# Kernel tuning notes

Measured on AMD Instinct MI355X. Metric: run time of the kernel, lower is better.

Reference implementation:

```python
import jax, jax.numpy as jnp
import numpy as np


def setup_inputs() -> dict:
    key = jax.random.key(0)
    ks = jax.random.split(key, 5)
    B, T, I, H = 32, 2048, 512, 512
    s_i = 1.0 / np.sqrt(I)
    s_h = 1.0 / np.sqrt(H)
    return {
        "x": jax.random.normal(ks[0], (B, T, I), dtype=jnp.float32),
        "Wi": jax.random.normal(ks[1], (4 * H, I), dtype=jnp.float32) * s_i,
        "bi": jax.random.normal(ks[2], (4 * H,), dtype=jnp.float32) * s_i,
        "Wh": jax.random.normal(ks[3], (4 * H, H), dtype=jnp.float32) * s_h,
        "bh": jax.random.normal(ks[4], (4 * H,), dtype=jnp.float32) * s_h,
    }


def reference(x, Wi, bi, Wh, bh):
    # x: [B, T, I] (batch_first). Wi: [4H, I], Wh: [4H, H].
    B, T, I = x.shape
    H = Wh.shape[1]
    # Precompute input contribution for all timesteps in one GEMM: [T, B, 4H]
    gx = jnp.einsum('bti,gi->tbg', x, Wi) + bi + bh

    def step(carry, g):
        h, c = carry
        gates = g + h @ Wh.T  # [B, 4H]
        i_g, f_g, c_g, o_g = jnp.split(gates, 4, axis=1)
        c_new = jax.nn.sigmoid(f_g) * c + jax.nn.sigmoid(i_g) * jnp.tanh(c_g)
        h_new = jax.nn.sigmoid(o_g) * jnp.tanh(c_new)
        return (h_new, c_new), h_new

    h0 = jnp.zeros((B, H), dtype=x.dtype)
    c0 = jnp.zeros((B, H), dtype=x.dtype)
    (h_fin, c_fin), ys = jax.lax.scan(step, (h0, c0), gx)
    output = ys.transpose(1, 0, 2)  # [B, T, H] (batch_first)
    return output, h_fin, c_fin
```

## Files before the change

kernel.cpp:

```cpp
#include <hip/hip_runtime.h>
#include <hip/hip_bf16.h>

typedef unsigned short ushort_t;
typedef __attribute__((ext_vector_type(8))) short bf16x8;
typedef __attribute__((ext_vector_type(4))) float f32x4;
typedef __attribute__((ext_vector_type(2))) float f32x2;

#define B_SZ 32
#define T_SZ 2048
#define I_SZ 512
#define H_SZ 512
#define G_SZ 2048
#define T_C  64
#define N_CHUNK (T_SZ / T_C)

__device__ __forceinline__ ushort_t f2bf(float f) {
    union { float f; unsigned u32; } c; c.f = f;
    unsigned r = c.u32 + 0x7fffu + ((c.u32 >> 16) & 1u);
    return (ushort_t)(r >> 16);
}
__device__ __forceinline__ bf16x8 cvt8(const float* __restrict__ p) {
    f32x4 a = *(const f32x4*)p;
    f32x4 b = *(const f32x4*)(p + 4);
    bf16x8 v;
    v[0] = (short)f2bf(a[0]); v[1] = (short)f2bf(a[1]);
    v[2] = (short)f2bf(a[2]); v[3] = (short)f2bf(a[3]);
    v[4] = (short)f2bf(b[0]); v[5] = (short)f2bf(b[1]);
    v[6] = (short)f2bf(b[2]); v[7] = (short)f2bf(b[3]);
    return v;
}
__device__ __forceinline__ float sigf(float x) { return 1.0f / (1.0f + __expf(-x)); }
__device__ __forceinline__ float tanh_fast(float x) {
    float a = fabsf(x);
    float e = __expf(-2.0f * a);
    float t = (1.0f - e) / (1.0f + e);
    return x < 0.0f ? -t : t;
}

__global__ __launch_bounds__(256) void gemm_gx(
    const float* __restrict__ X,
    const float* __restrict__ Wi,
    const float* __restrict__ bi,
    const float* __restrict__ bh,
    float* __restrict__ gx,
    int t0)
{
    __shared__ ushort_t As[128][40];
    __shared__ ushort_t Bs[128][40];

    const int tid  = threadIdx.x;
    const int lane = tid & 63;
    const int wv   = tid >> 6;
    const int wm   = (wv >> 1) * 64;
    const int wn   = (wv & 1) * 64;
    const int m0   = blockIdx.y * 128;
    const int n0   = blockIdx.x * 128;

    f32x4 acc[4][4];
#pragma unroll
    for (int i = 0; i < 4; i++)
#pragma unroll
        for (int j = 0; j < 4; j++) acc[i][j] = (f32x4)0.0f;

    const int lrow   = tid >> 2;
    const int lchunk = (tid & 3) * 8;

    const int m1 = m0 + lrow, m2 = m1 + 64;
    const size_t xr1 = ((size_t)(m1 >> 6) * T_SZ + t0 + (m1 & (T_C - 1))) * 512;
    const size_t xr2 = ((size_t)(m2 >> 6) * T_SZ + t0 + (m2 & (T_C - 1))) * 512;

    for (int kk = 0; kk < 512; kk += 32) {
        *(bf16x8*)&As[lrow][lchunk]      = cvt8(X + xr1 + kk + lchunk);
        *(bf16x8*)&As[lrow + 64][lchunk] = cvt8(X + xr2 + kk + lchunk);
        const float* bp = Wi + (size_t)(n0 + lrow) * 512 + kk + lchunk;
        *(bf16x8*)&Bs[lrow][lchunk]      = cvt8(bp);
        *(bf16x8*)&Bs[lrow + 64][lchunk] = cvt8(bp + (size_t)64 * 512);
        __syncthreads();

        const int koff = (lane >> 4) * 8;
        const int rsel = lane & 15;
        bf16x8 af[4], bfr[4];
#pragma unroll
        for (int mt = 0; mt < 4; mt++) af[mt]  = *(const bf16x8*)&As[wm + mt * 16 + rsel][koff];
#pragma unroll
        for (int nt = 0; nt < 4; nt++) bfr[nt] = *(const bf16x8*)&Bs[wn + nt * 16 + rsel][koff];
#pragma unroll
        for (int mt = 0; mt < 4; mt++)
#pragma unroll
            for (int nt = 0; nt < 4; nt++)
                acc[mt][nt] = __builtin_amdgcn_mfma_f32_16x16x32_bf16(af[mt], bfr[nt], acc[mt][nt], 0, 0, 0);
        __syncthreads();
    }

    const int rsel = lane & 15;
    const int rq   = (lane >> 4) * 4;
#pragma unroll
    for (int nt = 0; nt < 4; nt++) {
        const int n = n0 + wn + nt * 16 + rsel;
        const float bias = bi[n] + bh[n];
#pragma unroll
        for (int mt = 0; mt < 4; mt++) {
#pragma unroll
            for (int r = 0; r < 4; r++) {
                const int m  = m0 + wm + mt * 16 + rq + r;
                const int b  = m >> 6;
                const int tc = m & (T_C - 1);
                gx[((size_t)tc * B_SZ + b) * G_SZ + n] = acc[mt][nt][r] + bias;
            }
        }
    }
}

__global__ __launch_bounds__(256) void lstm_scan(
    const float* __restrict__ Wh,
    const float* __restrict__ gx,
    float* __restrict__ out,
    ushort_t* __restrict__ hstate,
    float*    __restrict__ cstate,
    unsigned* __restrict__ flags,
    int t0)
{
    const int w    = blockIdx.x;
    const int hb   = w * 16;
    const int tid  = threadIdx.x;
    const int lane = tid & 63;
    const int g    = tid >> 6;
    const int rsel = lane & 15;
    const int quad = lane >> 4;

    __shared__ float gs[4][32][16];

    bf16x8 bfrag[16];
    {
        const float* wp = Wh + (size_t)(g * 512 + hb + rsel) * 512 + quad * 8;
#pragma unroll
        for (int kt = 0; kt < 16; kt++) bfrag[kt] = cvt8(wp + kt * 32);
    }

    const int eb = tid >> 3;
    const int eh = (tid & 7) * 2;
    const size_t cidx = (size_t)eb * 512 + hb + eh;
    float c0 = 0.0f, c1 = 0.0f;
    if (t0 > 0) { c0 = cstate[cidx]; c1 = cstate[cidx + 1]; }
    float h0 = 0.0f, h1 = 0.0f;
    const size_t out_base = (size_t)eb * (T_SZ * H_SZ) + hb + eh;

    for (int tl = 0; tl < T_C; tl++) {
        const int t = t0 + tl;

        float gl0[4], gl1[4];
        {
            const float* gp = gx + (size_t)tl * (B_SZ * G_SZ) + (size_t)(g * 512 + hb + rsel);
#pragma unroll
            for (int r = 0; r < 4; r++) {
                const int b0 = quad * 4 + r;
                gl0[r] = gp[(size_t)b0 * G_SZ];
                gl1[r] = gp[(size_t)(b0 + 16) * G_SZ];
            }
        }
        __builtin_amdgcn_sched_barrier(0);

        if (t > 0) {
            const unsigned tgt = (unsigned)t;
            for (;;) {
                unsigned f = __hip_atomic_load(&flags[(lane & 31) * 32],
                                               __ATOMIC_RELAXED, __HIP_MEMORY_SCOPE_AGENT);
                if (__all((int)(f >= tgt))) break;
            }
            __builtin_amdgcn_fence(__ATOMIC_ACQUIRE, "agent");
        }

        f32x4 acc0a = (f32x4)0.0f, acc0b = (f32x4)0.0f;
        f32x4 acc1a = (f32x4)0.0f, acc1b = (f32x4)0.0f;
        if (t > 0) {
            const ushort_t* hp = hstate + (size_t)(t & 1) * (B_SZ * H_SZ)
                                 + (size_t)rsel * 512 + quad * 8;
#pragma unroll
            for (int kt = 0; kt < 16; kt += 2) {
                bf16x8 a0 = *(const bf16x8*)(hp + kt * 32);
                bf16x8 a1 = *(const bf16x8*)(hp + (size_t)16 * 512 + kt * 32);
                bf16x8 a2 = *(const bf16x8*)(hp + (kt + 1) * 32);
                bf16x8 a3 = *(const bf16x8*)(hp + (size_t)16 * 512 + (kt + 1) * 32);
                acc0a = __builtin_amdgcn_mfma_f32_16x16x32_bf16(a0, bfrag[kt],     acc0a, 0, 0, 0);
                acc1a = __builtin_amdgcn_mfma_f32_16x16x32_bf16(a1, bfrag[kt],     acc1a, 0, 0, 0);
                acc0b = __builtin_amdgcn_mfma_f32_16x16x32_bf16(a2, bfrag[kt + 1], acc0b, 0, 0, 0);
                acc1b = __builtin_amdgcn_mfma_f32_16x16x32_bf16(a3, bfrag[kt + 1], acc1b, 0, 0, 0);
            }
        }
        const f32x4 acc0 = acc0a + acc0b;
        const f32x4 acc1 = acc1a + acc1b;

#pragma unroll
        for (int r = 0; r < 4; r++) {
            const int b0 = quad * 4 + r;
            gs[g][b0][rsel]      = acc0[r] + gl0[r];
            gs[g][b0 + 16][rsel] = acc1[r] + gl1[r];
        }
        __syncthreads();

        {
            const float ig0 = gs[0][eb][eh], ig1 = gs[0][eb][eh + 1];
            const float fg0 = gs[1][eb][eh], fg1 = gs[1][eb][eh + 1];
            const float cg0 = gs[2][eb][eh], cg1 = gs[2][eb][eh + 1];
            const float og0 = gs[3][eb][eh], og1 = gs[3][eb][eh + 1];
            c0 = sigf(fg0) * c0 + sigf(ig0) * tanh_fast(cg0);
            c1 = sigf(fg1) * c1 + sigf(ig1) * tanh_fast(cg1);
            h0 = sigf(og0) * tanh_fast(c0);
            h1 = sigf(og1) * tanh_fast(c1);
            const unsigned hpack = (unsigned)f2bf(h0) | ((unsigned)f2bf(h1) << 16);
            ushort_t* wrp = hstate + (size_t)((t + 1) & 1) * (B_SZ * H_SZ) + cidx;
            __hip_atomic_store((unsigned*)wrp, hpack, __ATOMIC_RELAXED, __HIP_MEMORY_SCOPE_AGENT);
        }
        __syncthreads();

        if (tid == 0)
            __hip_atomic_store(&flags[w * 32], (unsigned)(t + 1),
                               __ATOMIC_RELEASE, __HIP_MEMORY_SCOPE_AGENT);

        f32x2 ho; ho[0] = h0; ho[1] = h1;
        *(f32x2*)(out + out_base + (size_t)t * H_SZ) = ho;
    }

    cstate[cidx] = c0; cstate[cidx + 1] = c1;
    if (t0 + T_C == T_SZ) {
        float* hf = out + (size_t)B_SZ * T_SZ * H_SZ;
        f32x2 hv; hv[0] = h0; hv[1] = h1;
        *(f32x2*)(hf + cidx) = hv;
        float* cf = hf + B_SZ * H_SZ;
        f32x2 cv; cv[0] = c0; cv[1] = c1;
        *(f32x2*)(cf + cidx) = cv;
    }
}

extern "C" void kernel_launch(void* const* d_in, const int* in_sizes, int n_in,
                              void* d_out, int out_size, void* d_ws, size_t ws_size,
                              hipStream_t stream) {
    const float* x  = (const float*)d_in[0];
    const float* Wi = (const float*)d_in[1];
    const float* bi = (const float*)d_in[2];
    const float* Wh = (const float*)d_in[3];
    const float* bh = (const float*)d_in[4];
    float* out = (float*)d_out;

    const size_t GX_BYTES = (size_t)T_C * B_SZ * G_SZ * sizeof(float);
    float*    gxc    = (float*)d_ws;
    ushort_t* hstate = (ushort_t*)((char*)d_ws + GX_BYTES);
    float*    cstate = (float*)   ((char*)d_ws + GX_BYTES + 65536);
    unsigned* flags  = (unsigned*)((char*)d_ws + GX_BYTES + 65536 + 65536);

    hipMemsetAsync(flags, 0, 4096, stream);

    for (int k = 0; k < N_CHUNK; k++) {
        const int t0 = k * T_C;
        gemm_gx<<<dim3(G_SZ / 128, (B_SZ * T_C) / 128), dim3(256), 0, stream>>>(
            x, Wi, bi, bh, gxc, t0);
        lstm_scan<<<dim3(32), dim3(256), 0, stream>>>(Wh, gxc, out, hstate, cstate, flags, t0);
    }
}
```

Before: 14.25 ms.

## Give each scan wave all four gates to drop block barriers and LDS exchange

The recurrent scan is reorganised so that each wavefront holds the Wh fragments for all four gates of its 16 hidden units and half of the batch. The gate nonlinearities can then run directly on MFMA accumulators, with no shared-memory transpose and no __syncthreads. Each wave now publishes its own progress flag, which gives 64 per-wave flags across 16 workgroups instead of 32 per-block flags. In exchange, register pressure grows to 64 bf16x8 fragments per thread, and h stores become 16-bit scalar atomics with less coalesced output writes.

```diff
diff --git a/kernel.cpp b/kernel.cpp
--- a/kernel.cpp
+++ b/kernel.cpp
@@ -13,6 +13,7 @@
 #define G_SZ 2048
 #define T_C  64
 #define N_CHUNK (T_SZ / T_C)
+#define NWG_SCAN 16
 
 __device__ __forceinline__ ushort_t f2bf(float f) {
     union { float f; unsigned u32; } c; c.f = f;
@@ -111,7 +112,7 @@
     }
 }
 
-__global__ __launch_bounds__(256) void lstm_scan(
+__global__ __launch_bounds__(256, 1) void lstm_scan(
     const float* __restrict__ Wh,
     const float* __restrict__ gx,
     float* __restrict__ out,
@@ -120,115 +121,104 @@
     unsigned* __restrict__ flags,
     int t0)
 {
-    const int w    = blockIdx.x;
-    const int hb   = w * 16;
-    const int tid  = threadIdx.x;
-    const int lane = tid & 63;
-    const int g    = tid >> 6;
-    const int rsel = lane & 15;
-    const int quad = lane >> 4;
-
-    __shared__ float gs[4][32][16];
-
-    bf16x8 bfrag[16];
-    {
+    const int w     = blockIdx.x;
+    const int tid   = threadIdx.x;
+    const int lane  = tid & 63;
+    const int v     = tid >> 6;
+    const int bhalf = v & 1;
+    const int hb    = w * 32 + (v >> 1) * 16;
+    const int rsel  = lane & 15;
+    const int quad  = lane >> 4;
+    const int wvid  = w * 4 + v;
+
+    bf16x8 bfrag[4][16];
+#pragma unroll
+    for (int g = 0; g < 4; g++) {
         const float* wp = Wh + (size_t)(g * 512 + hb + rsel) * 512 + quad * 8;
 #pragma unroll
-        for (int kt = 0; kt < 16; kt++) bfrag[kt] = cvt8(wp + kt * 32);
-    }
-
-    const int eb = tid >> 3;
-    const int eh = (tid & 7) * 2;
-    const size_t cidx = (size_t)eb * 512 + hb + eh;
-    float c0 = 0.0f, c1 = 0.0f;
-    if (t0 > 0) { c0 = cstate[cidx]; c1 = cstate[cidx + 1]; }
-    float h0 = 0.0f, h1 = 0.0f;
-    const size_t out_base = (size_t)eb * (T_SZ * H_SZ) + hb + eh;
+        for (int kt = 0; kt < 16; kt++) bfrag[g][kt] = cvt8(wp + kt * 32);
+    }
+
+    const int bb = bhalf * 16 + quad * 4;
+    float c[4] = {0.f, 0.f, 0.f, 0.f};
+    float hn[4] = {0.f, 0.f, 0.f, 0.f};
+    if (t0 > 0) {
+#pragma unroll
+        for (int r = 0; r < 4; r++) c[r] = cstate[(size_t)(bb + r) * 512 + hb + rsel];
+    }
 
     for (int tl = 0; tl < T_C; tl++) {
         const int t = t0 + tl;
 
-        float gl0[4], gl1[4];
+        float gl[4][4];
         {
-            const float* gp = gx + (size_t)tl * (B_SZ * G_SZ) + (size_t)(g * 512 + hb + rsel);
-#pragma unroll
-            for (int r = 0; r < 4; r++) {
-                const int b0 = quad * 4 + r;
-                gl0[r] = gp[(size_t)b0 * G_SZ];
-                gl1[r] = gp[(size_t)(b0 + 16) * G_SZ];
-            }
+            const float* gp = gx + (size_t)tl * (B_SZ * G_SZ) + hb + rsel;
+#pragma unroll
+            for (int g = 0; g < 4; g++)
+#pragma unroll
+                for (int r = 0; r < 4; r++)
+                    gl[g][r] = gp[(size_t)(bb + r) * G_SZ + g * 512];
         }
         __builtin_amdgcn_sched_barrier(0);
 
         if (t > 0) {
             const unsigned tgt = (unsigned)t;
             for (;;) {
-                unsigned f = __hip_atomic_load(&flags[(lane & 31) * 32],
+                unsigned f = __hip_atomic_load(&flags[lane * 32],
                                                __ATOMIC_RELAXED, __HIP_MEMORY_SCOPE_AGENT);
                 if (__all((int)(f >= tgt))) break;
             }
             __builtin_amdgcn_fence(__ATOMIC_ACQUIRE, "agent");
         }
 
-        f32x4 acc0a = (f32x4)0.0f, acc0b = (f32x4)0.0f;
-        f32x4 acc1a = (f32x4)0.0f, acc1b = (f32x4)0.0f;
+        f32x4 acc[4];
+#pragma unroll
+        for (int g = 0; g < 4; g++) acc[g] = (f32x4)0.0f;
         if (t > 0) {
             const ushort_t* hp = hstate + (size_t)(t & 1) * (B_SZ * H_SZ)
-                                 + (size_t)rsel * 512 + quad * 8;
-#pragma unroll
-            for (int kt = 0; kt < 16; kt += 2) {
-                bf16x8 a0 = *(const bf16x8*)(hp + kt * 32);
-                bf16x8 a1 = *(const bf16x8*)(hp + (size_t)16 * 512 + kt * 32);
-                bf16x8 a2 = *(const bf16x8*)(hp + (kt + 1) * 32);
-                bf16x8 a3 = *(const bf16x8*)(hp + (size_t)16 * 512 + (kt + 1) * 32);
-                acc0a = __builtin_amdgcn_mfma_f32_16x16x32_bf16(a0, bfrag[kt],     acc0a, 0, 0, 0);
-                acc1a = __builtin_amdgcn_mfma_f32_16x16x32_bf16(a1, bfrag[kt],     acc1a, 0, 0, 0);
-                acc0b = __builtin_amdgcn_mfma_f32_16x16x32_bf16(a2, bfrag[kt + 1], acc0b, 0, 0, 0);
-                acc1b = __builtin_amdgcn_mfma_f32_16x16x32_bf16(a3, bfrag[kt + 1], acc1b, 0, 0, 0);
+                                 + (size_t)(bhalf * 16 + rsel) * 512 + quad * 8;
+#pragma unroll
+            for (int kt = 0; kt < 16; kt++) {
+                bf16x8 a = *(const bf16x8*)(hp + kt * 32);
+                acc[0] = __builtin_amdgcn_mfma_f32_16x16x32_bf16(a, bfrag[0][kt], acc[0], 0, 0, 0);
+                acc[1] = __builtin_amdgcn_mfma_f32_16x16x32_bf16(a, bfrag[1][kt], acc[1], 0, 0, 0);
+                acc[2] = __builtin_amdgcn_mfma_f32_16x16x32_bf16(a, bfrag[2][kt], acc[2], 0, 0, 0);
+                acc[3] = __builtin_amdgcn_mfma_f32_16x16x32_bf16(a, bfrag[3][kt], acc[3], 0, 0, 0);
             }
         }
-        const f32x4 acc0 = acc0a + acc0b;
-        const f32x4 acc1 = acc1a + acc1b;
-
+
+        ushort_t* hw = hstate + (size_t)((t + 1) & 1) * (B_SZ * H_SZ);
 #pragma unroll
         for (int r = 0; r < 4; r++) {
-            const int b0 = quad * 4 + r;
-            gs[g][b0][rsel]      = acc0[r] + gl0[r];
-            gs[g][b0 + 16][rsel] = acc1[r] + gl1[r];
-        }
-        __syncthreads();
-
-        {
-            const float ig0 = gs[0][eb][eh], ig1 = gs[0][eb][eh + 1];
-            const float fg0 = gs[1][eb][eh], fg1 = gs[1][eb][eh + 1];
-            const float cg0 = gs[2][eb][eh], cg1 = gs[2][eb][eh + 1];
-            const float og0 = gs[3][eb][eh], og1 = gs[3][eb][eh + 1];
-            c0 = sigf(fg0) * c0 + sigf(ig0) * tanh_fast(cg0);
-            c1 = sigf(fg1) * c1 + sigf(ig1) * tanh_fast(cg1);
-            h0 = sigf(og0) * tanh_fast(c0);
-            h1 = sigf(og1) * tanh_fast(c1);
-            const unsigned hpack = (unsigned)f2bf(h0) | ((unsigned)f2bf(h1) << 16);
-            ushort_t* wrp = hstate + (size_t)((t + 1) & 1) * (B_SZ * H_SZ) + cidx;
-            __hip_atomic_store((unsigned*)wrp, hpack, __ATOMIC_RELAXED, __HIP_MEMORY_SCOPE_AGENT);
-        }
-        __syncthreads();
-
-        if (tid == 0)
-            __hip_atomic_store(&flags[w * 32], (unsigned)(t + 1),
+            const float ig = acc[0][r] + gl[0][r];
+            const float fg = acc[1][r] + gl[1][r];
+            const float cg = acc[2][r] + gl[2][r];
+            const float og = acc[3][r] + gl[3][r];
+            c[r]  = sigf(fg) * c[r] + sigf(ig) * tanh_fast(cg);
+            hn[r] = sigf(og) * tanh_fast(c[r]);
+            __hip_atomic_store(&hw[(size_t)(bb + r) * 512 + hb + rsel], f2bf(hn[r]),
+                               __ATOMIC_RELAXED, __HIP_MEMORY_SCOPE_AGENT);
+        }
+
+        if (lane == 0)
+            __hip_atomic_store(&flags[wvid * 32], (unsigned)(t + 1),
                                __ATOMIC_RELEASE, __HIP_MEMORY_SCOPE_AGENT);
 
-        f32x2 ho; ho[0] = h0; ho[1] = h1;
-        *(f32x2*)(out + out_base + (size_t)t * H_SZ) = ho;
-    }
-
-    cstate[cidx] = c0; cstate[cidx + 1] = c1;
+#pragma unroll
+        for (int r = 0; r < 4; r++)
+            out[(size_t)(bb + r) * (T_SZ * H_SZ) + (size_t)t * H_SZ + hb + rsel] = hn[r];
+    }
+
+#pragma unroll
+    for (int r = 0; r < 4; r++) cstate[(size_t)(bb + r) * 512 + hb + rsel] = c[r];
     if (t0 + T_C == T_SZ) {
         float* hf = out + (size_t)B_SZ * T_SZ * H_SZ;
-        f32x2 hv; hv[0] = h0; hv[1] = h1;
-        *(f32x2*)(hf + cidx) = hv;
         float* cf = hf + B_SZ * H_SZ;
-        f32x2 cv; cv[0] = c0; cv[1] = c1;
-        *(f32x2*)(cf + cidx) = cv;
+#pragma unroll
+        for (int r = 0; r < 4; r++) {
+            hf[(size_t)(bb + r) * 512 + hb + rsel] = hn[r];
+            cf[(size_t)(bb + r) * 512 + hb + rsel] = c[r];
+        }
     }
 }
 
@@ -248,12 +238,12 @@
     float*    cstate = (float*)   ((char*)d_ws + GX_BYTES + 65536);
     unsigned* flags  = (unsigned*)((char*)d_ws + GX_BYTES + 65536 + 65536);
 
-    hipMemsetAsync(flags, 0, 4096, stream);
+    hipMemsetAsync(flags, 0, 8192, stream);
 
     for (int k = 0; k < N_CHUNK; k++) {
         const int t0 = k * T_C;
         gemm_gx<<<dim3(G_SZ / 128, (B_SZ * T_C) / 128), dim3(256), 0, stream>>>(
             x, Wi, bi, bh, gxc, t0);
-        lstm_scan<<<dim3(32), dim3(256), 0, stream>>>(Wh, gxc, out, hstate, cstate, flags, t0);
-    }
-}
+        lstm_scan<<<dim3(NWG_SCAN), dim3(256), 0, stream>>>(Wh, gxc, out, hstate, cstate, flags, t0);
+    }
+}
```

Result: slower. 18.01 ms (+26.4%).

## Double-buffer gate LDS and compute cell update redundantly per wave to drop barrier

Applied to the files above, without the earlier changes.

Gate pre-activations go to a double-buffered shared array laid out as f32x4 in the MFMA output layout. Every wave then reads all four gates for its own (batch, hidden) fragment and repeats the cell update, so the second __syncthreads per timestep goes away. Only wave 0 writes h (bf16 stores, one per element), the output and the state. The intent is a shorter serial critical path per step, paid for with four-fold redundant transcendental math, narrower scattered global stores, and a larger flags memset.

```diff
diff --git a/kernel.cpp b/kernel.cpp
--- a/kernel.cpp
+++ b/kernel.cpp
@@ -128,7 +128,7 @@
     const int rsel = lane & 15;
     const int quad = lane >> 4;
 
-    __shared__ float gs[4][32][16];
+    __shared__ f32x4 gs2[2][4][8][16];
 
     bf16x8 bfrag[16];
     {
@@ -137,16 +137,22 @@
         for (int kt = 0; kt < 16; kt++) bfrag[kt] = cvt8(wp + kt * 32);
     }
 
-    const int eb = tid >> 3;
-    const int eh = (tid & 7) * 2;
-    const size_t cidx = (size_t)eb * 512 + hb + eh;
-    float c0 = 0.0f, c1 = 0.0f;
-    if (t0 > 0) { c0 = cstate[cidx]; c1 = cstate[cidx + 1]; }
-    float h0 = 0.0f, h1 = 0.0f;
-    const size_t out_base = (size_t)eb * (T_SZ * H_SZ) + hb + eh;
+    float c[2][4], hn[2][4];
+#pragma unroll
+    for (int hf = 0; hf < 2; hf++)
+#pragma unroll
+        for (int r = 0; r < 4; r++) { c[hf][r] = 0.0f; hn[hf][r] = 0.0f; }
+    if (t0 > 0) {
+#pragma unroll
+        for (int hf = 0; hf < 2; hf++)
+#pragma unroll
+            for (int r = 0; r < 4; r++)
+                c[hf][r] = cstate[(size_t)(quad * 4 + r + 16 * hf) * 512 + hb + rsel];
+    }
 
     for (int tl = 0; tl < T_C; tl++) {
         const int t = t0 + tl;
+        const int p = t & 1;
 
         float gl0[4], gl1[4];
         {
@@ -173,7 +179,7 @@
         f32x4 acc0a = (f32x4)0.0f, acc0b = (f32x4)0.0f;
         f32x4 acc1a = (f32x4)0.0f, acc1b = (f32x4)0.0f;
         if (t > 0) {
-            const ushort_t* hp = hstate + (size_t)(t & 1) * (B_SZ * H_SZ)
+            const ushort_t* hp = hstate + (size_t)p * (B_SZ * H_SZ)
                                  + (size_t)rsel * 512 + quad * 8;
 #pragma unroll
             for (int kt = 0; kt < 16; kt += 2) {
@@ -190,45 +196,71 @@
         const f32x4 acc0 = acc0a + acc0b;
         const f32x4 acc1 = acc1a + acc1b;
 
-#pragma unroll
-        for (int r = 0; r < 4; r++) {
-            const int b0 = quad * 4 + r;
-            gs[g][b0][rsel]      = acc0[r] + gl0[r];
-            gs[g][b0 + 16][rsel] = acc1[r] + gl1[r];
+        {
+            f32x4 w0, w1;
+#pragma unroll
+            for (int r = 0; r < 4; r++) { w0[r] = acc0[r] + gl0[r]; w1[r] = acc1[r] + gl1[r]; }
+            gs2[p][g][quad][rsel]     = w0;
+            gs2[p][g][quad + 4][rsel] = w1;
         }
         __syncthreads();
 
-        {
-            const float ig0 = gs[0][eb][eh], ig1 = gs[0][eb][eh + 1];
-            const float fg0 = gs[1][eb][eh], fg1 = gs[1][eb][eh + 1];
-            const float cg0 = gs[2][eb][eh], cg1 = gs[2][eb][eh + 1];
-            const float og0 = gs[3][eb][eh], og1 = gs[3][eb][eh + 1];
-            c0 = sigf(fg0) * c0 + sigf(ig0) * tanh_fast(cg0);
-            c1 = sigf(fg1) * c1 + sigf(ig1) * tanh_fast(cg1);
-            h0 = sigf(og0) * tanh_fast(c0);
-            h1 = sigf(og1) * tanh_fast(c1);
-            const unsigned hpack = (unsigned)f2bf(h0) | ((unsigned)f2bf(h1) << 16);
-            ushort_t* wrp = hstate + (size_t)((t + 1) & 1) * (B_SZ * H_SZ) + cidx;
-            __hip_atomic_store((unsigned*)wrp, hpack, __ATOMIC_RELAXED, __HIP_MEMORY_SCOPE_AGENT);
-        }
-        __syncthreads();
+#pragma unroll
+        for (int hf = 0; hf < 2; hf++) {
+            const f32x4 vi = gs2[p][0][quad + 4 * hf][rsel];
+            const f32x4 vf = gs2[p][1][quad + 4 * hf][rsel];
+            const f32x4 vc = gs2[p][2][quad + 4 * hf][rsel];
+            const f32x4 vo = gs2[p][3][quad + 4 * hf][rsel];
+#pragma unroll
+            for (int r = 0; r < 4; r++) {
+                c[hf][r]  = sigf(vf[r]) * c[hf][r] + sigf(vi[r]) * tanh_fast(vc[r]);
+                hn[hf][r] = sigf(vo[r]) * tanh_fast(c[hf][r]);
+            }
+        }
+
+        if (g == 0) {
+            ushort_t* hw = hstate + (size_t)((t + 1) & 1) * (B_SZ * H_SZ);
+#pragma unroll
+            for (int hf = 0; hf < 2; hf++)
+#pragma unroll
+                for (int r = 0; r < 4; r++)
+                    __hip_atomic_store(&hw[(size_t)(quad * 4 + r + 16 * hf) * 512 + hb + rsel],
+                                       f2bf(hn[hf][r]),
+                                       __ATOMIC_RELAXED, __HIP_MEMORY_SCOPE_AGENT);
+        }
 
         if (tid == 0)
             __hip_atomic_store(&flags[w * 32], (unsigned)(t + 1),
                                __ATOMIC_RELEASE, __HIP_MEMORY_SCOPE_AGENT);
 
-        f32x2 ho; ho[0] = h0; ho[1] = h1;
-        *(f32x2*)(out + out_base + (size_t)t * H_SZ) = ho;
-    }
-
-    cstate[cidx] = c0; cstate[cidx + 1] = c1;
-    if (t0 + T_C == T_SZ) {
-        float* hf = out + (size_t)B_SZ * T_SZ * H_SZ;
-        f32x2 hv; hv[0] = h0; hv[1] = h1;
-        *(f32x2*)(hf + cidx) = hv;
-        float* cf = hf + B_SZ * H_SZ;
-        f32x2 cv; cv[0] = c0; cv[1] = c1;
-        *(f32x2*)(cf + cidx) = cv;
+        if (g == 0) {
+#pragma unroll
+            for (int hf = 0; hf < 2; hf++)
+#pragma unroll
+                for (int r = 0; r < 4; r++)
+                    out[(size_t)(quad * 4 + r + 16 * hf) * (T_SZ * H_SZ)
+                        + (size_t)t * H_SZ + hb + rsel] = hn[hf][r];
+        }
+    }
+
+    if (g == 0) {
+#pragma unroll
+        for (int hf = 0; hf < 2; hf++)
+#pragma unroll
+            for (int r = 0; r < 4; r++)
+                cstate[(size_t)(quad * 4 + r + 16 * hf) * 512 + hb + rsel] = c[hf][r];
+        if (t0 + T_C == T_SZ) {
+            float* hf_ = out + (size_t)B_SZ * T_SZ * H_SZ;
+            float* cf_ = hf_ + B_SZ * H_SZ;
+#pragma unroll
+            for (int hf = 0; hf < 2; hf++)
+#pragma unroll
+                for (int r = 0; r < 4; r++) {
+                    const size_t idx = (size_t)(quad * 4 + r + 16 * hf) * 512 + hb + rsel;
+                    hf_[idx] = hn[hf][r];
+                    cf_[idx] = c[hf][r];
+                }
+        }
     }
 }
 
@@ -248,7 +280,7 @@
     float*    cstate = (float*)   ((char*)d_ws + GX_BYTES + 65536);
     unsigned* flags  = (unsigned*)((char*)d_ws + GX_BYTES + 65536 + 65536);
 
-    hipMemsetAsync(flags, 0, 4096, stream);
+    hipMemsetAsync(flags, 0, 8192, stream);
 
     for (int k = 0; k < N_CHUNK; k++) {
         const int t0 = k * T_C;
```

New measurement: 17.19 ms. 1.21x slower.
